# Performance work log

Measured on AMD Instinct MI355X. Metric: run time of the kernel, lower is better.

## Reference

```python
import jax, jax.numpy as jnp
import numpy as np


def setup_inputs() -> dict:
    key = jax.random.key(0)
    k1, k2, k3 = jax.random.split(key, 3)
    B, D, F, P = 4096, 1024, 2048, 1024
    return {
        "x": jax.random.normal(k1, (B, D), dtype=jnp.float32),
        "features": jax.random.normal(k2, (F, D), dtype=jnp.float32),
        "prototypes": jax.random.normal(k3, (P, D), dtype=jnp.float32),
        "alpha": jnp.ones((1,), dtype=jnp.float32),
        "beta": jnp.ones((1,), dtype=jnp.float32),
        "theta": jnp.ones((1,), dtype=jnp.float32),
    }


def reference(x, features, prototypes, alpha, beta, theta):
    # Project each set ONCE (the original redundantly broadcasts first).
    xf = x @ features.T            # [B, F]
    pf = prototypes @ features.T   # [P, F]
    sx = jax.nn.sigmoid(xf)        # x_present [B, F]
    sp = jax.nn.sigmoid(pf)        # p_present [P, F]
    ax = xf * sx                   # [B, F]
    bp = pf * sp                   # [P, F]
    # common[b,p]        = sum_f xf*pf*sx*sp            = (xf*sx) @ (pf*sp)^T
    # x_distinct[b,p]    = sum_f xf*sx*(1-sp)           = rowsum(xf*sx) - (xf*sx) @ sp^T
    # p_distinct[b,p]    = sum_f pf*sp*(1-sx)           = rowsum(pf*sp) - sx @ (pf*sp)^T
    common = ax @ bp.T                                     # [B, P]
    x_distinctive = ax.sum(axis=1, keepdims=True) - ax @ sp.T  # [B, P]
    p_distinctive = bp.sum(axis=1)[None, :] - sx @ bp.T        # [B, P]
    return theta * common - alpha * x_distinctive - beta * p_distinctive
```

## Files before the change

kernel.cpp:

```cpp
#include <hip/hip_runtime.h>
#include <hip/hip_bf16.h>

typedef __bf16 bf16_t;
typedef bf16_t bf16x4 __attribute__((ext_vector_type(4)));
typedef bf16_t bf16x8 __attribute__((ext_vector_type(8)));
typedef float f32x4 __attribute__((ext_vector_type(4)));

#define AS1 __attribute__((address_space(1)))
#define AS3 __attribute__((address_space(3)))

__device__ __forceinline__ void gload_lds16(const void* g, void* l) {
    __builtin_amdgcn_global_load_lds((const AS1 void*)g, (AS3 void*)l, 16, 0, 0);
}
__device__ __forceinline__ void gload_lds4(const void* g, void* l) {
    __builtin_amdgcn_global_load_lds((const AS1 void*)g, (AS3 void*)l, 4, 0, 0);
}

__device__ __forceinline__ float sigmoidf_(float v) {
    return 1.0f / (1.0f + __expf(-v));
}

__global__ __launch_bounds__(256) void k_convert3(const float* __restrict__ x,
                                                  const float* __restrict__ pr,
                                                  const float* __restrict__ ft,
                                                  bf16_t* __restrict__ dst) {
    const int n4 = 7168 * 256;
    int i = blockIdx.x * 256 + threadIdx.x;
    const int stride = gridDim.x * 256;
    for (; i < n4; i += stride) {
        float4 v;
        if (i < 1048576) v = ((const float4*)x)[i];
        else if (i < 1310720) v = ((const float4*)pr)[i - 1048576];
        else v = ((const float4*)ft)[i - 1310720];
        bf16x4 o;
        o[0] = (bf16_t)v.x; o[1] = (bf16_t)v.y; o[2] = (bf16_t)v.z; o[3] = (bf16_t)v.w;
        ((bf16x4*)dst)[i] = o;
    }
}

__global__ __launch_bounds__(256) void k_foldrs(const float* __restrict__ rsPart,
                                                float* __restrict__ rsums) {
    const int r = blockIdx.x * 256 + threadIdx.x;
    float s = 0.f;
#pragma unroll
    for (int b = 0; b < 8; ++b) s += rsPart[b * 5120 + r];
    rsums[r] = s;
}

__global__ __launch_bounds__(256) void k_reduce4(const bf16_t* __restrict__ part,
                                                 const float* __restrict__ rsums,
                                                 const float* __restrict__ pa,
                                                 float* __restrict__ out) {
    const int idx = blockIdx.x * 256 + threadIdx.x;
    const int region = idx >> 13;
    const int widx = idx & 8191;
    const int wv = widx >> 10;
    const int chunk = (widx >> 6) & 15;
    const int ln = widx & 63;
    const int bx = region >> 2, by = region & 3;
    const int wm = wv >> 2, wn = wv & 3;
    const int fg = chunk >> 1, gp = chunk & 1;
    const int er = (ln >> 4) << 2, ec = ln & 15;
    const long off = (long)idx * 8;

    float sum[8] = {};
#pragma unroll
    for (int s = 0; s < 4; ++s) {
        bf16x8 v = *(const bf16x8*)(part + (long)s * 4194304 + off);
#pragma unroll
        for (int j = 0; j < 8; ++j) sum[j] += (float)v[j];
    }
    const int r0 = bx * 256 + wm * 128 + fg * 16 + er;
    const int c0 = by * 256 + wn * 64 + gp * 32 + ec;
    const float a = pa[0];
#pragma unroll
    for (int q = 0; q < 4; ++q) {
        const float ra = a * rsums[r0 + q];
#pragma unroll
        for (int gh = 0; gh < 2; ++gh) {
            const int c = c0 + gh * 16;
            out[(long)(r0 + q) * 1024 + c] = sum[gh * 4 + q] - ra - rsums[4096 + c];
        }
    }
}

__global__ __launch_bounds__(512, 2) void gemm2_8p(
    const bf16_t* __restrict__ A, const bf16_t* __restrict__ B,
    int NT, long ldab, long ldbb, bf16_t* __restrict__ O1, long zstride) {
    __shared__ char lds[131072];
    const int tid = threadIdx.x;
    const int wave = tid >> 6, lane = tid & 63;
    const int wm = wave >> 2, wn = wave & 3;

    const int gx = gridDim.x, gy = gridDim.y;
    const int o = blockIdx.x + gx * (blockIdx.y + gy * blockIdx.z);
    const int cpx = (gx * gy * (int)gridDim.z) >> 3;
    const int v = (o & 7) * cpx + (o >> 3);
    const int bx = v % gx;
    const int rem = v / gx;
    const int by = rem % gy;
    const int bz = rem / gy;

    const long bm = (long)bx * 256, bn = (long)by * 256;
    const int kb0 = bz * NT * 64;
    const char* Ab = (const char*)A + bm * ldab;
    const char* Bb = (const char*)B + bn * ldbb;

    const int swzcb = ((lane >> 4) << 4) ^ (((lane >> 3) & 1) << 5);
    const int base_a = (wm * 128 + (lane & 15)) * 64 + swzcb;
    const int base_b = (wn * 64 + (lane & 15)) * 64 + swzcb;

    f32x4 acc[8][4] = {};

    auto STAGE = [&](const char* gb, long ld, int kbyte, int ldsoff) {
#pragma unroll
        for (int j = 0; j < 2; ++j) {
            const int oo = (j * 512 + tid) << 4;
            const int r = oo >> 6;
            const int cb = (oo & 63) ^ (((oo >> 9) & 1) << 5);
            gload_lds16(gb + (long)r * ld + kbyte + cb, lds + ldsoff + (oo & ~1023));
        }
    };

#define VM8 asm volatile("s_waitcnt vmcnt(8)" ::: "memory")
#define VM4 asm volatile("s_waitcnt vmcnt(4)" ::: "memory")
#define VM0 asm volatile("s_waitcnt vmcnt(0)" ::: "memory")

    auto PFETCH = [&](int pf) {
        const int kbyte = (kb0 + pf * 32) * 2;
        const int ps = pf & 3;
        STAGE(Ab, ldab, kbyte, ps * 16384);
        STAGE(Bb, ldbb, kbyte, 65536 + ps * 16384);
    };

#define PHASE2(p, WAITSTMT, DOPF)                                               \
    do {                                                                        \
        WAITSTMT;                                                               \
        __builtin_amdgcn_s_barrier();                                           \
        const int slot = (p) & 3;                                               \
        const char* sA = lds + slot * 16384;                                    \
        const char* sB = lds + 65536 + slot * 16384;                            \
        bf16x8 af[8];                                                           \
        bf16x8 bfr[4];                                                          \
        _Pragma("unroll") for (int f = 0; f < 8; ++f)                           \
            af[f] = *(const bf16x8*)(sA + base_a + f * 1024);                   \
        _Pragma("unroll") for (int g = 0; g < 4; ++g)                           \
            bfr[g] = *(const bf16x8*)(sB + base_b + g * 1024);                  \
        if (DOPF) PFETCH((p) + 3);                                              \
        __builtin_amdgcn_sched_barrier(0);                                      \
        __builtin_amdgcn_s_setprio(1);                                          \
        _Pragma("unroll") for (int f = 0; f < 8; ++f)                           \
            _Pragma("unroll") for (int g = 0; g < 4; ++g)                       \
                acc[f][g] = __builtin_amdgcn_mfma_f32_16x16x32_bf16(            \
                    af[f], bfr[g], acc[f][g], 0, 0, 0);                         \
        __builtin_amdgcn_s_setprio(0);                                          \
        __builtin_amdgcn_sched_barrier(0);                                      \
    } while (0)

    const int NP = NT * 2;
    PFETCH(0);
    PFETCH(1);
    PFETCH(2);

    for (int p = 0; p < NP - 3; ++p) PHASE2(p, VM8, 1);
    PHASE2(NP - 3, VM8, 0);
    PHASE2(NP - 2, VM4, 0);
    PHASE2(NP - 1, VM0, 0);

#undef PHASE2
#undef VM8
#undef VM4
#undef VM0

    bf16_t* Op = O1 + (long)bz * zstride + (long)(bx * 4 + by) * 65536 +
                 wave * 8192 + lane * 8;
#pragma unroll
    for (int fg = 0; fg < 8; ++fg)
#pragma unroll
        for (int gp = 0; gp < 2; ++gp) {
            bf16x8 w;
#pragma unroll
            for (int gh = 0; gh < 2; ++gh)
#pragma unroll
                for (int q = 0; q < 4; ++q)
                    w[gh * 4 + q] = (bf16_t)acc[fg][gp * 2 + gh][q];
            *(bf16x8*)(Op + (fg * 2 + gp) * 512) = w;
        }
}

__global__ __launch_bounds__(512, 2) void gemm1_160(
    const bf16_t* __restrict__ A, const bf16_t* __restrict__ B,
    bf16_t* __restrict__ O1, bf16_t* __restrict__ O1b,
    float* __restrict__ rsPart,
    const float* __restrict__ pa, const float* __restrict__ pb,
    const float* __restrict__ pt) {
    __shared__ char lds[106496];
    const int tid = threadIdx.x;
    const int wave = tid >> 6, lane = tid & 63;
    const int wm = wave >> 2, wn = wave & 3;
    const int NT = 16;

    const int gx = gridDim.x, gy = gridDim.y;
    const int o = blockIdx.x + gx * blockIdx.y;
    const int cpx = (gx * gy) >> 3;
    const int v = (o & 7) * cpx + (o >> 3);
    const int bx = v % gx;
    const int by = v / gx;

    const long bm = (long)bx * 160, bn = (long)by * 256;
    const char* Ab = (const char*)A + bm * 2048;
    const char* Bb = (const char*)B + bn * 2048;

    const int swzcb = ((lane >> 4) << 4) ^ (((lane >> 3) & 1) << 5);
    const int base_a = (wm * 80 + (lane & 15)) * 64 + swzcb;
    const int base_b = (wn * 64 + (lane & 15)) * 64 + swzcb;

    f32x4 acc[5][4] = {};

    auto STAGE_A = [&](int kbyte, int ldsoff) {
        {
            const int oo = tid << 4;
            const int r = oo >> 6;
            const int cb = (oo & 63) ^ (((oo >> 9) & 1) << 5);
            gload_lds16(Ab + (long)r * 2048 + kbyte + cb, lds + ldsoff + (oo & ~1023));
        }
        {
            const int oo = 8192 + (tid << 2);
            const int r = oo >> 6;
            const int cb = (oo & 63) ^ (((oo >> 9) & 1) << 5);
            gload_lds4(Ab + (long)r * 2048 + kbyte + cb, lds + ldsoff + 8192 + wave * 256);
        }
    };
    auto STAGE_B = [&](int kbyte, int ldsoff) {
#pragma unroll
        for (int j = 0; j < 2; ++j) {
            const int oo = (j * 512 + tid) << 4;
            const int r = oo >> 6;
            const int cb = (oo & 63) ^ (((oo >> 9) & 1) << 5);
            gload_lds16(Bb + (long)r * 2048 + kbyte + cb, lds + ldsoff + (oo & ~1023));
        }
    };

#define VM8 asm volatile("s_waitcnt vmcnt(8)" ::: "memory")
#define VM4 asm volatile("s_waitcnt vmcnt(4)" ::: "memory")
#define VM0 asm volatile("s_waitcnt vmcnt(0)" ::: "memory")

    auto PFETCH = [&](int pf) {
        const int kbyte = pf * 64;
        const int ps = pf & 3;
        STAGE_A(kbyte, ps * 10240);
        STAGE_B(kbyte, 40960 + ps * 16384);
    };

#define PHASE1(p, WAITSTMT, DOPF)                                               \
    do {                                                                        \
        WAITSTMT;                                                               \
        __builtin_amdgcn_s_barrier();                                           \
        const int slot = (p) & 3;                                               \
        const char* sA = lds + slot * 10240;                                    \
        const char* sB = lds + 40960 + slot * 16384;                            \
        bf16x8 af[5];                                                           \
        bf16x8 bfr[4];                                                          \
        _Pragma("unroll") for (int f = 0; f < 5; ++f)                           \
            af[f] = *(const bf16x8*)(sA + base_a + f * 1024);                   \
        _Pragma("unroll") for (int g = 0; g < 4; ++g)                           \
            bfr[g] = *(const bf16x8*)(sB + base_b + g * 1024);                  \
        if (DOPF) PFETCH((p) + 3);                                              \
        __builtin_amdgcn_sched_barrier(0);                                      \
        __builtin_amdgcn_s_setprio(1);                                          \
        _Pragma("unroll") for (int f = 0; f < 5; ++f)                           \
            _Pragma("unroll") for (int g = 0; g < 4; ++g)                       \
                acc[f][g] = __builtin_amdgcn_mfma_f32_16x16x32_bf16(            \
                    bfr[g], af[f], acc[f][g], 0, 0, 0);                         \
        __builtin_amdgcn_s_setprio(0);                                          \
        __builtin_amdgcn_sched_barrier(0);                                      \
    } while (0)

    const int NP = NT * 2;
    PFETCH(0);
    PFETCH(1);
    PFETCH(2);

    for (int p = 0; p < NP - 3; ++p) PHASE1(p, VM8, 1);
    PHASE1(NP - 3, VM8, 0);
    PHASE1(NP - 2, VM4, 0);
    PHASE1(NP - 1, VM0, 0);

#undef PHASE1
#undef VM8
#undef VM4
#undef VM0

    __syncthreads();

    const float va = pa[0], vb = pb[0], vt = pt[0];
    const int lm = lane & 15;
    const int ln4 = (lane >> 4) << 2;
    char* wlds = lds + 4096 + wave * 4096;
    const int wswz = (lm & 7) << 4;
    float rs[5];
#pragma unroll
    for (int f = 0; f < 5; ++f) rs[f] = 0.f;

#pragma unroll
    for (int mf = 0; mf < 5; ++mf) {
        const long growbase = bm + wm * 80 + mf * 16;
        const bool isXf = (growbase < 4096);
        bf16_t* gb = isXf ? O1 : O1b;
        const long rbase0 = isXf ? growbase : (growbase - 4096);
#pragma unroll
        for (int g = 0; g < 4; ++g) {
            bf16x4 w0, w1;
#pragma unroll
            for (int q = 0; q < 4; ++q) {
                const float vv = acc[mf][g][q];
                const float s = sigmoidf_(vv);
                const float prod = vv * s;
                w0[q] = (bf16_t)(isXf ? prod : (vt * prod + va * s));
                w1[q] = (bf16_t)(isXf ? s : (vb * prod));
                rs[mf] += isXf ? prod : vb * prod;
            }
            const int a = lm * 128 + ((g * 32 + ln4 * 2) ^ wswz);
            *(bf16x4*)(wlds + a) = w0;
            *(bf16x4*)(wlds + 2048 + a) = w1;
        }
#pragma unroll
        for (int rd = 0; rd < 2; ++rd) {
            const int row = rd * 8 + (lane >> 3);
            const int a = row * 128 + (((lane & 7) * 16) ^ ((row & 7) << 4));
            bf16x8 v0 = *(const bf16x8*)(wlds + a);
            bf16x8 v1 = *(const bf16x8*)(wlds + 2048 + a);
            bf16_t* dst = gb + (rbase0 + row) * 4096 + bn + wn * 64 + (lane & 7) * 8;
            *(bf16x8*)dst = v0;
            *(bf16x8*)(dst + 2048) = v1;
        }
    }

    float* lds_f = (float*)lds;
#pragma unroll
    for (int f = 0; f < 5; ++f) {
        float t = rs[f];
        t += __shfl_xor(t, 16);
        t += __shfl_xor(t, 32);
        if ((lane >> 4) == 0) lds_f[wn * 160 + wm * 80 + f * 16 + lm] = t;
    }
    __syncthreads();
    if (tid < 160) {
        const float s = lds_f[tid] + lds_f[160 + tid] + lds_f[320 + tid] + lds_f[480 + tid];
        rsPart[(long)by * 5120 + bm + tid] = s;
    }
}

extern "C" void kernel_launch(void* const* d_in, const int* in_sizes, int n_in,
                              void* d_out, int out_size, void* d_ws, size_t ws_size,
                              hipStream_t stream) {
    const float* x = (const float*)d_in[0];
    const float* feats = (const float*)d_in[1];
    const float* protos = (const float*)d_in[2];
    const float* pa = (const float*)d_in[3];
    const float* pb = (const float*)d_in[4];
    const float* pt = (const float*)d_in[5];
    float* out = (float*)d_out;

    constexpr long Bsz = 4096, D = 1024, F = 2048, P = 1024;

    bf16_t* XP = (bf16_t*)d_ws;
    bf16_t* F16 = XP + (Bsz + P) * D;
    bf16_t* A2 = F16 + F * D;
    bf16_t* B2 = A2 + Bsz * 2 * F;
    float* rsums = (float*)(B2 + P * 2 * F);
    bf16_t* part = (bf16_t*)(rsums + Bsz + P);
    float* rsPart = (float*)(part + 4L * Bsz * P);

    k_convert3<<<2048, 256, 0, stream>>>(x, protos, feats, XP);

    gemm1_160<<<dim3(32, 8), 512, 0, stream>>>(XP, F16, A2, B2, rsPart, pa, pb, pt);

    k_foldrs<<<20, 256, 0, stream>>>(rsPart, rsums);

    gemm2_8p<<<dim3(Bsz / 256, P / 256, 4), 512, 0, stream>>>(
        A2, B2, (int)(2 * F / 64 / 4), 2 * F * 2, 2 * F * 2, part, (long)Bsz * P);

    k_reduce4<<<2048, 256, 0, stream>>>(part, rsums, pa, out);
}
```

Before: 92.51 us.

## Store gemm1 outputs in K-blocked layout for contiguous gemm2 tile loads

gemm1 now writes its sigmoid-derived operands directly into a K-blocked layout (32-element K chunks, rows contiguous within each chunk). It drops the LDS staging transpose before the global stores. gemm2 then loads each 256x32 tile as one contiguous 16 KB region instead of strided rows, which should improve load coalescing and simplify address math. The trade-off is that gemm1's global stores become scattered 8-byte writes, which may cost more write efficiency than the gemm2 loads gain.

```diff
diff --git a/kernel.cpp b/kernel.cpp
--- a/kernel.cpp
+++ b/kernel.cpp
@@ -85,8 +85,8 @@
 }
 
 __global__ __launch_bounds__(512, 2) void gemm2_8p(
-    const bf16_t* __restrict__ A, const bf16_t* __restrict__ B,
-    int NT, long ldab, long ldbb, bf16_t* __restrict__ O1, long zstride) {
+    const bf16_t* __restrict__ A2s, const bf16_t* __restrict__ B2s,
+    bf16_t* __restrict__ O1, long zstride) {
     __shared__ char lds[131072];
     const int tid = threadIdx.x;
     const int wave = tid >> 6, lane = tid & 63;
@@ -102,9 +102,9 @@
     const int bz = rem / gy;
 
     const long bm = (long)bx * 256, bn = (long)by * 256;
-    const int kb0 = bz * NT * 64;
-    const char* Ab = (const char*)A + bm * ldab;
-    const char* Bb = (const char*)B + bn * ldbb;
+    const int kb32_0 = bz * 32;
+    const char* Ab = (const char*)A2s;
+    const char* Bb = (const char*)B2s;
 
     const int swzcb = ((lane >> 4) << 4) ^ (((lane >> 3) & 1) << 5);
     const int base_a = (wm * 128 + (lane & 15)) * 64 + swzcb;
@@ -112,13 +112,12 @@
 
     f32x4 acc[8][4] = {};
 
-    auto STAGE = [&](const char* gb, long ld, int kbyte, int ldsoff) {
+    auto STAGEC = [&](const char* gbase, int ldsoff) {
 #pragma unroll
         for (int j = 0; j < 2; ++j) {
             const int oo = (j * 512 + tid) << 4;
-            const int r = oo >> 6;
             const int cb = (oo & 63) ^ (((oo >> 9) & 1) << 5);
-            gload_lds16(gb + (long)r * ld + kbyte + cb, lds + ldsoff + (oo & ~1023));
+            gload_lds16(gbase + (oo & ~63) + cb, lds + ldsoff + (oo & ~1023));
         }
     };
 
@@ -127,10 +126,10 @@
 #define VM0 asm volatile("s_waitcnt vmcnt(0)" ::: "memory")
 
     auto PFETCH = [&](int pf) {
-        const int kbyte = (kb0 + pf * 32) * 2;
+        const long kb = kb32_0 + pf;
         const int ps = pf & 3;
-        STAGE(Ab, ldab, kbyte, ps * 16384);
-        STAGE(Bb, ldbb, kbyte, 65536 + ps * 16384);
+        STAGEC(Ab + (kb * 4096 + bm) * 64, ps * 16384);
+        STAGEC(Bb + (kb * 1024 + bn) * 64, 65536 + ps * 16384);
     };
 
 #define PHASE2(p, WAITSTMT, DOPF)                                               \
@@ -157,7 +156,7 @@
         __builtin_amdgcn_sched_barrier(0);                                      \
     } while (0)
 
-    const int NP = NT * 2;
+    const int NP = 32;
     PFETCH(0);
     PFETCH(1);
     PFETCH(2);
@@ -190,7 +189,7 @@
 
 __global__ __launch_bounds__(512, 2) void gemm1_160(
     const bf16_t* __restrict__ A, const bf16_t* __restrict__ B,
-    bf16_t* __restrict__ O1, bf16_t* __restrict__ O1b,
+    bf16_t* __restrict__ A2s, bf16_t* __restrict__ B2s,
     float* __restrict__ rsPart,
     const float* __restrict__ pa, const float* __restrict__ pb,
     const float* __restrict__ pt) {
@@ -291,26 +290,25 @@
 #undef VM4
 #undef VM0
 
-    __syncthreads();
-
     const float va = pa[0], vb = pb[0], vt = pt[0];
     const int lm = lane & 15;
     const int ln4 = (lane >> 4) << 2;
-    char* wlds = lds + 4096 + wave * 4096;
-    const int wswz = (lm & 7) << 4;
+    const int kbbase = (int)(bn >> 5) + wn * 2;
     float rs[5];
 #pragma unroll
     for (int f = 0; f < 5; ++f) rs[f] = 0.f;
 
 #pragma unroll
     for (int mf = 0; mf < 5; ++mf) {
-        const long growbase = bm + wm * 80 + mf * 16;
-        const bool isXf = (growbase < 4096);
-        bf16_t* gb = isXf ? O1 : O1b;
-        const long rbase0 = isXf ? growbase : (growbase - 4096);
+        const long grow = bm + wm * 80 + mf * 16 + lm;
+        const bool isXf = (grow < 4096);
+        const long rowidx = isXf ? grow : (grow - 4096);
+        const long rowsz = isXf ? 4096 : 1024;
+        bf16_t* base = isXf ? A2s : B2s;
 #pragma unroll
         for (int g = 0; g < 4; ++g) {
             bf16x4 w0, w1;
+            float rsl = 0.f;
 #pragma unroll
             for (int q = 0; q < 4; ++q) {
                 const float vv = acc[mf][g][q];
@@ -318,24 +316,17 @@
                 const float prod = vv * s;
                 w0[q] = (bf16_t)(isXf ? prod : (vt * prod + va * s));
                 w1[q] = (bf16_t)(isXf ? s : (vb * prod));
-                rs[mf] += isXf ? prod : vb * prod;
+                rsl += isXf ? prod : vb * prod;
             }
-            const int a = lm * 128 + ((g * 32 + ln4 * 2) ^ wswz);
-            *(bf16x4*)(wlds + a) = w0;
-            *(bf16x4*)(wlds + 2048 + a) = w1;
-        }
-#pragma unroll
-        for (int rd = 0; rd < 2; ++rd) {
-            const int row = rd * 8 + (lane >> 3);
-            const int a = row * 128 + (((lane & 7) * 16) ^ ((row & 7) << 4));
-            bf16x8 v0 = *(const bf16x8*)(wlds + a);
-            bf16x8 v1 = *(const bf16x8*)(wlds + 2048 + a);
-            bf16_t* dst = gb + (rbase0 + row) * 4096 + bn + wn * 64 + (lane & 7) * 8;
-            *(bf16x8*)dst = v0;
-            *(bf16x8*)(dst + 2048) = v1;
-        }
-    }
-
+            rs[mf] += rsl;
+            const long kb = kbbase + (g >> 1);
+            const int c0 = (g & 1) * 16 + ln4;
+            *(bf16x4*)(base + (kb * rowsz + rowidx) * 32 + c0) = w0;
+            *(bf16x4*)(base + ((kb + 64) * rowsz + rowidx) * 32 + c0) = w1;
+        }
+    }
+
+    __syncthreads();
     float* lds_f = (float*)lds;
 #pragma unroll
     for (int f = 0; f < 5; ++f) {
@@ -366,20 +357,20 @@
 
     bf16_t* XP = (bf16_t*)d_ws;
     bf16_t* F16 = XP + (Bsz + P) * D;
-    bf16_t* A2 = F16 + F * D;
-    bf16_t* B2 = A2 + Bsz * 2 * F;
-    float* rsums = (float*)(B2 + P * 2 * F);
+    bf16_t* A2s = F16 + F * D;
+    bf16_t* B2s = A2s + Bsz * 2 * F;
+    float* rsums = (float*)(B2s + P * 2 * F);
     bf16_t* part = (bf16_t*)(rsums + Bsz + P);
     float* rsPart = (float*)(part + 4L * Bsz * P);
 
     k_convert3<<<2048, 256, 0, stream>>>(x, protos, feats, XP);
 
-    gemm1_160<<<dim3(32, 8), 512, 0, stream>>>(XP, F16, A2, B2, rsPart, pa, pb, pt);
+    gemm1_160<<<dim3(32, 8), 512, 0, stream>>>(XP, F16, A2s, B2s, rsPart, pa, pb, pt);
 
     k_foldrs<<<20, 256, 0, stream>>>(rsPart, rsums);
 
     gemm2_8p<<<dim3(Bsz / 256, P / 256, 4), 512, 0, stream>>>(
-        A2, B2, (int)(2 * F / 64 / 4), 2 * F * 2, 2 * F * 2, part, (long)Bsz * P);
+        A2s, B2s, part, (long)Bsz * P);
 
     k_reduce4<<<2048, 256, 0, stream>>>(part, rsums, pa, out);
 }
```

Measured after the change: 89.80 us. 1.03x faster.
